# Kernel tuning notes

Hardware: AMD Instinct MI355X
Metric: run time of the kernel (lower is better)

Reference implementation:

```python
import jax, jax.numpy as jnp
import numpy as np

EPS = 0.1
TANH_SCALE = 1.0
B, T, N, D, C, DE = 8, 120, 24, 48, 1128, 256  # C = D*(D-1)//2


def setup_inputs() -> dict:
    key = jax.random.key(0)
    k1, k2, k3, k4 = jax.random.split(key, 4)
    x = jax.random.normal(k1, (B, T, N, D), dtype=jnp.float32)
    context = jax.random.normal(k2, (B, C, N, DE), dtype=jnp.float32)
    Wkv = jax.random.normal(k3, (D, DE), dtype=jnp.float32) * (DE ** -0.5)
    bkv = jax.random.normal(k4, (D,), dtype=jnp.float32) * 0.01
    return {"x": x, "context": context, "Wkv": Wkv, "bkv": bkv}


def reference(x, context, Wkv, bkv):
    # x: [B,T,N,D], context: [B,C,N,DE]
    b, t, n, d = x.shape
    kv = jnp.einsum('bcne,de->bcnd', context, Wkv) + bkv      # [B,C,N,D]
    kv = jnp.transpose(kv, (0, 2, 3, 1))                      # [B,N,D,C]
    xt = jnp.transpose(x, (0, 2, 1, 3))                       # [B,N,T,D]
    sp = jnp.einsum('bntd,bndc->bntc', xt, kv)                # [B,N,T,C]
    sp = EPS * TANH_SCALE * jnp.tanh(sp / TANH_SCALE)
    i, j = jnp.tril_indices(d, k=-1)
    A = jnp.zeros((b, n, t, d, d), dtype=x.dtype).at[..., i, j].set(sp)
    A = A - jnp.swapaxes(A, -1, -2)                           # skew-symmetric
    dx = jnp.einsum('bntd,bntde->bnte', xt, A)                # per-(B,N,T) matvec
    y = xt + dx
    return jnp.transpose(y, (0, 2, 1, 3))                     # [B,T,N,D]
```

## Files before the change

### kernel.cpp

```cpp
#include <hip/hip_runtime.h>
#include <hip/hip_bf16.h>


constexpr int Bc = 8, Tc = 120, Nc = 24, Dc = 48, Cc = 1128, DEc = 256;
constexpr int BNc = Bc * Nc;
constexpr int KVP = 48;

using short8 = __attribute__((ext_vector_type(8))) short;
using f32x4  = __attribute__((ext_vector_type(4))) float;

__device__ __forceinline__ ushort f2b(float f) {
    union { float f; unsigned u; } v; v.f = f;
    unsigned r = (v.u + 0x7fffu + ((v.u >> 16) & 1u)) >> 16;
    return (ushort)r;
}
__device__ __forceinline__ float b2f(ushort u) {
    union { unsigned q; float f; } cv; cv.q = ((unsigned)u) << 16; return cv.f;
}
__device__ __forceinline__ short bcast(float f) {
    return (short)__bfloat16_as_ushort(__float2bfloat16(f));
}
__device__ __forceinline__ short8 pack8(const float4& a, const float4& b) {
    short8 r;
    r[0] = bcast(a.x); r[1] = bcast(a.y); r[2] = bcast(a.z); r[3] = bcast(a.w);
    r[4] = bcast(b.x); r[5] = bcast(b.y); r[6] = bcast(b.z); r[7] = bcast(b.w);
    return r;
}

constexpr int SWs = 264;
__global__ __launch_bounds__(256) void k1_kv(const float* __restrict__ ctx,
                                             const float* __restrict__ Wkv,
                                             const float* __restrict__ bkv,
                                             ushort* __restrict__ kvb) {
    __shared__ ushort sW[Dc * SWs];
    const int bn = blockIdx.x, c0 = blockIdx.y * 128;
    const int b = bn / Nc, n = bn % Nc;
    const int tid = threadIdx.x, wave = tid >> 6, lane = tid & 63;
    const int tr = lane & 15, kg = lane >> 4;
    const float* ctxb = ctx + ((size_t)b * Cc * Nc + n) * DEc;

    for (int l = tid; l < Dc * 64; l += 256) {
        int d = l >> 6, e = (l & 63) << 2;
        float4 w = *reinterpret_cast<const float4*>(Wkv + d * DEc + e);
        ushort4 u;
        u.x = (ushort)bcast(w.x); u.y = (ushort)bcast(w.y);
        u.z = (ushort)bcast(w.z); u.w = (ushort)bcast(w.w);
        *reinterpret_cast<ushort4*>(&sW[d * SWs + e]) = u;
    }

    const float* crow[2];
    #pragma unroll
    for (int cn = 0; cn < 2; ++cn) {
        int c = c0 + wave * 32 + cn * 16 + tr;
        crow[cn] = ctxb + (size_t)(c < Cc ? c : Cc - 1) * (Nc * DEc);
    }

    f32x4 acc[3][2];
    #pragma unroll
    for (int mf = 0; mf < 3; ++mf)
        #pragma unroll
        for (int cn = 0; cn < 2; ++cn) acc[mf][cn] = (f32x4){0.f, 0.f, 0.f, 0.f};

    __syncthreads();

    #pragma unroll
    for (int ks = 0; ks < 8; ++ks) {
        const int e0 = ks * 32 + kg * 8;
        short8 bfrag[2];
        #pragma unroll
        for (int cn = 0; cn < 2; ++cn) {
            float4 a0 = *reinterpret_cast<const float4*>(crow[cn] + e0);
            float4 a1 = *reinterpret_cast<const float4*>(crow[cn] + e0 + 4);
            bfrag[cn] = pack8(a0, a1);
        }
        short8 afrag[3];
        #pragma unroll
        for (int mf = 0; mf < 3; ++mf)
            afrag[mf] = *reinterpret_cast<const short8*>(&sW[(mf * 16 + tr) * SWs + e0]);
        #pragma unroll
        for (int mf = 0; mf < 3; ++mf)
            #pragma unroll
            for (int cn = 0; cn < 2; ++cn)
                acc[mf][cn] = __builtin_amdgcn_mfma_f32_16x16x32_bf16(afrag[mf], bfrag[cn], acc[mf][cn], 0, 0, 0);
    }

    float4 bias[3];
    #pragma unroll
    for (int mf = 0; mf < 3; ++mf)
        bias[mf] = *reinterpret_cast<const float4*>(bkv + mf * 16 + kg * 4);
    #pragma unroll
    for (int cn = 0; cn < 2; ++cn) {
        int c = c0 + wave * 32 + cn * 16 + tr;
        if (c < Cc) {
            ushort* dst = kvb + ((size_t)bn * Cc + c) * KVP;
            #pragma unroll
            for (int mf = 0; mf < 3; ++mf) {
                ushort4 u;
                u.x = f2b(acc[mf][cn][0] + bias[mf].x);
                u.y = f2b(acc[mf][cn][1] + bias[mf].y);
                u.z = f2b(acc[mf][cn][2] + bias[mf].z);
                u.w = f2b(acc[mf][cn][3] + bias[mf].w);
                *reinterpret_cast<ushort4*>(dst + mf * 16 + kg * 4) = u;
            }
        }
    }
}

constexpr int SG2 = 1140;
__global__ __launch_bounds__(256, 3) void k2_fused(const float* __restrict__ x,
                                                   const ushort* __restrict__ kvb,
                                                   float* __restrict__ out) {
    __shared__ ushort sG[16 * SG2];
    __shared__ float  sXf[16 * 52];
    __shared__ ushort sXb[16 * 72];
    const int L = blockIdx.x;
    const int bn = (L & 7) + 8 * (L >> 6);
    const int tt = (L >> 3) & 7;
    const int b = bn / Nc, n = bn % Nc, t0 = tt * 16;
    const int tid = threadIdx.x, wave = tid >> 6, lane = tid & 63;
    const int tr = lane & 15, kg = lane >> 4;

    if (tid < 96) {
        int t = tid / 6, q = tid % 6;
        *reinterpret_cast<ushort4*>(&sXb[t * 72 + 48 + q * 4]) = make_ushort4(0, 0, 0, 0);
    }
    for (int l = tid; l < 16 * 12; l += 256)
        sG[(l / 12) * SG2 + 1128 + (l % 12)] = 0;
    if (tid < 192) {
        int t = tid / 12, dv = (tid % 12) * 4, tg = t0 + t;
        float4 v = make_float4(0.f, 0.f, 0.f, 0.f);
        if (tg < Tc) v = *reinterpret_cast<const float4*>(x + (((size_t)b * Tc + tg) * Nc + n) * Dc + dv);
        *reinterpret_cast<float4*>(&sXf[t * 52 + dv]) = v;
        *reinterpret_cast<ushort4*>(&sXb[t * 72 + dv]) = make_ushort4(f2b(v.x), f2b(v.y), f2b(v.z), f2b(v.w));
    }
    __syncthreads();
    const short8 af0 = *reinterpret_cast<const short8*>(&sXb[tr * 72 + kg * 8]);
    const short8 af1 = *reinterpret_cast<const short8*>(&sXb[tr * 72 + 32 + kg * 8]);

    const ushort* kvbn = kvb + (size_t)bn * Cc * KVP;
    short8 b0, b1, p0, p1;
    {
        int c = wave * 16 + tr;
        const ushort* p = kvbn + (size_t)c * KVP + kg * 8;
        b0 = *reinterpret_cast<const short8*>(p);
        b1 = *reinterpret_cast<const short8*>(p + 32);
    }
    #pragma unroll
    for (int u = 0; u < 18; ++u) {
        if (u < 17) {
            int c = (wave + (u + 1) * 4) * 16 + tr; if (c > Cc - 1) c = Cc - 1;
            const ushort* p = kvbn + (size_t)c * KVP + kg * 8;
            p0 = *reinterpret_cast<const short8*>(p);
            p1 = *reinterpret_cast<const short8*>(p + 32);
        }
        f32x4 a = (f32x4){0.f, 0.f, 0.f, 0.f};
        a = __builtin_amdgcn_mfma_f32_16x16x32_bf16(af0, b0, a, 0, 0, 0);
        a = __builtin_amdgcn_mfma_f32_16x16x32_bf16(af1, b1, a, 0, 0, 0);
        int c = (wave + u * 4) * 16 + tr;
        if (c < Cc) {
            #pragma unroll
            for (int r = 0; r < 4; ++r) {
                float g = 0.1f - 0.2f * __builtin_amdgcn_rcpf(__expf(2.0f * a[r]) + 1.0f);
                sG[(kg * 4 + r) * SG2 + c] = f2b(g);
            }
        }
        b0 = p0; b1 = p1;
    }
    __syncthreads();

    int ea[3], ta[3], tea[3];
    float dxa[3];
    #pragma unroll
    for (int p = 0; p < 3; ++p) {
        int idx = tid + p * 256;
        ta[p] = idx / 48; ea[p] = idx % 48;
        tea[p] = ea[p] * (ea[p] - 1) / 2;
        dxa[p] = 0.f;
    }
    int td = 0;
    #pragma unroll 4
    for (int d = 0; d < 48; ++d) {
        #pragma unroll
        for (int p = 0; p < 3; ++p) {
            bool gt = d > ea[p];
            int c = gt ? (td + ea[p]) : (tea[p] + d);
            float gv = b2f(sG[ta[p] * SG2 + c]);
            float xv = sXf[ta[p] * 52 + d];
            float m = gt ? xv : -xv;
            if (d == ea[p]) m = 0.f;
            dxa[p] = fmaf(m, gv, dxa[p]);
        }
        td += d;
    }
    #pragma unroll
    for (int p = 0; p < 3; ++p) {
        int tg = t0 + ta[p];
        if (tg < Tc)
            out[(((size_t)b * Tc + tg) * Nc + n) * Dc + ea[p]] = sXf[ta[p] * 52 + ea[p]] + dxa[p];
    }
}

extern "C" void kernel_launch(void* const* d_in, const int* in_sizes, int n_in,
                              void* d_out, int out_size, void* d_ws, size_t ws_size,
                              hipStream_t stream) {
    (void)in_sizes; (void)n_in; (void)out_size; (void)ws_size;
    const float* x   = (const float*)d_in[0];
    const float* ctx = (const float*)d_in[1];
    const float* Wkv = (const float*)d_in[2];
    const float* bkv = (const float*)d_in[3];
    float* out   = (float*)d_out;
    ushort* kvb  = (ushort*)d_ws;

    k1_kv<<<dim3(BNc, 9), dim3(256), 0, stream>>>(ctx, Wkv, bkv, kvb);
    k2_fused<<<dim3(BNc * 8), dim3(256), 0, stream>>>(x, kvb, out);
}
```

Measured before the change: 79.98 us.

## Process 30 time steps per block in fused kernel to halve kv reloads

The fused kernel now covers 30 time steps per block instead of 16, using two MFMA row tiles (16 plus 14 padded rows) against each loaded kv fragment. This halves the number of blocks and the number of times each (b,n) kv slice is read from global memory, and removes the padding waste from 120 not dividing by 16. In exchange the block uses more shared memory and registers, the launch bound drops to 2 blocks per CU, and the grid shrinks to 768 blocks, which may reduce latency hiding. The tail loop now handles 6 elements per thread with clamped indices.

```diff
diff --git a/kernel.cpp b/kernel.cpp
--- a/kernel.cpp
+++ b/kernel.cpp
@@ -106,36 +106,41 @@
     }
 }
 
+constexpr int TT4 = 30;
 constexpr int SG2 = 1140;
-__global__ __launch_bounds__(256, 3) void k2_fused(const float* __restrict__ x,
+__global__ __launch_bounds__(256, 2) void k2_fused(const float* __restrict__ x,
                                                    const ushort* __restrict__ kvb,
                                                    float* __restrict__ out) {
-    __shared__ ushort sG[16 * SG2];
-    __shared__ float  sXf[16 * 52];
-    __shared__ ushort sXb[16 * 72];
+    __shared__ ushort sG[TT4 * SG2];
+    __shared__ float  sXf[TT4 * 52];
+    __shared__ ushort sXb[32 * 72];
     const int L = blockIdx.x;
-    const int bn = (L & 7) + 8 * (L >> 6);
-    const int tt = (L >> 3) & 7;
-    const int b = bn / Nc, n = bn % Nc, t0 = tt * 16;
+    const int bn = (L & 7) + 8 * (L >> 5);
+    const int tt = (L >> 3) & 3;
+    const int b = bn / Nc, n = bn % Nc, t0 = tt * TT4;
     const int tid = threadIdx.x, wave = tid >> 6, lane = tid & 63;
     const int tr = lane & 15, kg = lane >> 4;
 
-    if (tid < 96) {
+    if (tid < 180) {
         int t = tid / 6, q = tid % 6;
         *reinterpret_cast<ushort4*>(&sXb[t * 72 + 48 + q * 4]) = make_ushort4(0, 0, 0, 0);
-    }
-    for (int l = tid; l < 16 * 12; l += 256)
+    } else if (tid < 198) {
+        int l = tid - 180;
+        *reinterpret_cast<short8*>(&sXb[30 * 72 + l * 8]) = (short8){0, 0, 0, 0, 0, 0, 0, 0};
+    }
+    for (int l = tid; l < TT4 * 12; l += 256)
         sG[(l / 12) * SG2 + 1128 + (l % 12)] = 0;
-    if (tid < 192) {
-        int t = tid / 12, dv = (tid % 12) * 4, tg = t0 + t;
-        float4 v = make_float4(0.f, 0.f, 0.f, 0.f);
-        if (tg < Tc) v = *reinterpret_cast<const float4*>(x + (((size_t)b * Tc + tg) * Nc + n) * Dc + dv);
+    for (int l = tid; l < TT4 * 12; l += 256) {
+        int t = l / 12, dv = (l % 12) * 4;
+        float4 v = *reinterpret_cast<const float4*>(x + (((size_t)b * Tc + t0 + t) * Nc + n) * Dc + dv);
         *reinterpret_cast<float4*>(&sXf[t * 52 + dv]) = v;
         *reinterpret_cast<ushort4*>(&sXb[t * 72 + dv]) = make_ushort4(f2b(v.x), f2b(v.y), f2b(v.z), f2b(v.w));
     }
     __syncthreads();
     const short8 af0 = *reinterpret_cast<const short8*>(&sXb[tr * 72 + kg * 8]);
     const short8 af1 = *reinterpret_cast<const short8*>(&sXb[tr * 72 + 32 + kg * 8]);
+    const short8 ag0 = *reinterpret_cast<const short8*>(&sXb[(16 + tr) * 72 + kg * 8]);
+    const short8 ag1 = *reinterpret_cast<const short8*>(&sXb[(16 + tr) * 72 + 32 + kg * 8]);
 
     const ushort* kvbn = kvb + (size_t)bn * Cc * KVP;
     short8 b0, b1, p0, p1;
@@ -153,26 +158,35 @@
             p0 = *reinterpret_cast<const short8*>(p);
             p1 = *reinterpret_cast<const short8*>(p + 32);
         }
-        f32x4 a = (f32x4){0.f, 0.f, 0.f, 0.f};
-        a = __builtin_amdgcn_mfma_f32_16x16x32_bf16(af0, b0, a, 0, 0, 0);
-        a = __builtin_amdgcn_mfma_f32_16x16x32_bf16(af1, b1, a, 0, 0, 0);
+        f32x4 alo = (f32x4){0.f, 0.f, 0.f, 0.f};
+        f32x4 ahi = (f32x4){0.f, 0.f, 0.f, 0.f};
+        alo = __builtin_amdgcn_mfma_f32_16x16x32_bf16(af0, b0, alo, 0, 0, 0);
+        alo = __builtin_amdgcn_mfma_f32_16x16x32_bf16(af1, b1, alo, 0, 0, 0);
+        ahi = __builtin_amdgcn_mfma_f32_16x16x32_bf16(ag0, b0, ahi, 0, 0, 0);
+        ahi = __builtin_amdgcn_mfma_f32_16x16x32_bf16(ag1, b1, ahi, 0, 0, 0);
         int c = (wave + u * 4) * 16 + tr;
         if (c < Cc) {
             #pragma unroll
             for (int r = 0; r < 4; ++r) {
-                float g = 0.1f - 0.2f * __builtin_amdgcn_rcpf(__expf(2.0f * a[r]) + 1.0f);
-                sG[(kg * 4 + r) * SG2 + c] = f2b(g);
+                int tl = kg * 4 + r;
+                float glo = 0.1f - 0.2f * __builtin_amdgcn_rcpf(__expf(2.0f * alo[r]) + 1.0f);
+                sG[tl * SG2 + c] = f2b(glo);
+                if (tl + 16 < TT4) {
+                    float ghi = 0.1f - 0.2f * __builtin_amdgcn_rcpf(__expf(2.0f * ahi[r]) + 1.0f);
+                    sG[(tl + 16) * SG2 + c] = f2b(ghi);
+                }
             }
         }
         b0 = p0; b1 = p1;
     }
     __syncthreads();
 
-    int ea[3], ta[3], tea[3];
-    float dxa[3];
-    #pragma unroll
-    for (int p = 0; p < 3; ++p) {
+    int ea[6], ta[6], tea[6];
+    float dxa[6];
+    #pragma unroll
+    for (int p = 0; p < 6; ++p) {
         int idx = tid + p * 256;
+        if (idx >= TT4 * 48) idx = TT4 * 48 - 1;
         ta[p] = idx / 48; ea[p] = idx % 48;
         tea[p] = ea[p] * (ea[p] - 1) / 2;
         dxa[p] = 0.f;
@@ -181,7 +195,7 @@
     #pragma unroll 4
     for (int d = 0; d < 48; ++d) {
         #pragma unroll
-        for (int p = 0; p < 3; ++p) {
+        for (int p = 0; p < 6; ++p) {
             bool gt = d > ea[p];
             int c = gt ? (td + ea[p]) : (tea[p] + d);
             float gv = b2f(sG[ta[p] * SG2 + c]);
@@ -193,10 +207,10 @@
         td += d;
     }
     #pragma unroll
-    for (int p = 0; p < 3; ++p) {
-        int tg = t0 + ta[p];
-        if (tg < Tc)
-            out[(((size_t)b * Tc + tg) * Nc + n) * Dc + ea[p]] = sXf[ta[p] * 52 + ea[p]] + dxa[p];
+    for (int p = 0; p < 6; ++p) {
+        int idx = tid + p * 256;
+        if (idx < TT4 * 48)
+            out[(((size_t)b * Tc + t0 + ta[p]) * Nc + n) * Dc + ea[p]] = sXf[ta[p] * 52 + ea[p]] + dxa[p];
     }
 }
 
@@ -212,5 +226,5 @@
     ushort* kvb  = (ushort*)d_ws;
 
     k1_kv<<<dim3(BNc, 9), dim3(256), 0, stream>>>(ctx, Wkv, bkv, kvb);
-    k2_fused<<<dim3(BNc * 8), dim3(256), 0, stream>>>(x, kvb, out);
-}
+    k2_fused<<<dim3(BNc * 4), dim3(256), 0, stream>>>(x, kvb, out);
+}
```

Result: slower. 85.92 us (+7.4%).
